# Performance work log

Measured on AMD Instinct MI355X. Metric: run time of the kernel, lower is better.

## Reference

```python
import jax, jax.numpy as jnp
import numpy as np

D_MODEL = 1024
N_HEADS = 16
D_K = D_MODEL // N_HEADS
MAX_REL = 128
SCALE = 1.0 / np.sqrt(D_K)
TEMP = 1.0


def setup_inputs() -> dict:
    key = jax.random.key(0)
    ks = jax.random.split(key, 12)
    B, S = 4, 1024
    inp = {
        "query": jax.random.normal(ks[0], (B, S, D_MODEL), jnp.float32),
        "key": jax.random.normal(ks[1], (B, S, D_MODEL), jnp.float32),
        "value": jax.random.normal(ks[2], (B, S, D_MODEL), jnp.float32),
        "mask": jnp.ones((B, S), jnp.int32),
        "w_q": jax.random.normal(ks[3], (D_MODEL, D_MODEL), jnp.float32) * 0.03,
        "b_q": jnp.zeros((D_MODEL,), jnp.float32),
        "w_k": jax.random.normal(ks[4], (D_MODEL, D_MODEL), jnp.float32) * 0.03,
        "b_k": jnp.zeros((D_MODEL,), jnp.float32),
        "w_v": jax.random.normal(ks[5], (D_MODEL, D_MODEL), jnp.float32) * 0.03,
        "b_v": jnp.zeros((D_MODEL,), jnp.float32),
        "w_o": jax.random.normal(ks[6], (D_MODEL, D_MODEL), jnp.float32) * 0.03,
        "b_o": jnp.zeros((D_MODEL,), jnp.float32),
        "rel_k": jax.random.normal(ks[7], (2 * MAX_REL + 1, D_K), jnp.float32),
        "rel_v": jax.random.normal(ks[8], (2 * MAX_REL + 1, D_K), jnp.float32),
    }
    return inp


def _relative_positions(seq_len):
    pos = jnp.arange(seq_len)
    rel = pos[None, :] - pos[:, None]  # [S, S]
    return jnp.clip(rel, -MAX_REL, MAX_REL) + MAX_REL


def reference(query, key, value, mask, w_q, b_q, w_k, b_k, w_v, b_v, w_o, b_o, rel_k, rel_v):
    B, S, _ = query.shape
    # projections (torch Linear: x @ W.T + b)
    Q = (query @ w_q.T + b_q).reshape(B, S, N_HEADS, D_K).transpose(0, 2, 1, 3)  # [B,H,S,d]
    K = (key @ w_k.T + b_k).reshape(B, S, N_HEADS, D_K).transpose(0, 2, 1, 3)
    V = (value @ w_v.T + b_v).reshape(B, S, N_HEADS, D_K).transpose(0, 2, 1, 3)

    scores = jnp.einsum("bhld,bhrd->bhlr", Q, K) * SCALE  # [B,H,S,S]

    rel_idx = _relative_positions(S)                      # [S,S] int
    rpk = rel_k[rel_idx]                                  # [S,S,d]
    scores = scores + jnp.einsum("bhld,lrd->bhlr", Q, rpk)

    scores = scores / TEMP
    m = mask[:, None, None, :]                            # [B,1,1,S]
    scores = jnp.where(m == 0, -1e9, scores)

    attn = jax.nn.softmax(scores, axis=-1)                # [B,H,S,S]
    context = jnp.einsum("bhlr,bhrd->bhld", attn, V)
    rpv = rel_v[rel_idx]                                  # [S,S,d]
    context = context + jnp.einsum("bhlr,lrd->bhld", attn, rpv)

    context = context.transpose(0, 2, 1, 3).reshape(B, S, D_MODEL)
    out = context @ w_o.T + b_o
    return out
```

## Files before the change

kernel.cpp:

```cpp
#include <hip/hip_runtime.h>
#include <hip/hip_bf16.h>

#define S_LEN  1024
#define DMODEL 1024
#define NHEADS 16
#define DK     64
#define SCALE  0.125f

typedef __bf16 bf16x8_t __attribute__((ext_vector_type(8)));
typedef __bf16 bf16x4_t __attribute__((ext_vector_type(4)));
typedef float  f32x4_t  __attribute__((ext_vector_type(4)));

#define MFMA16(A, B, C) __builtin_amdgcn_mfma_f32_16x16x32_bf16((A), (B), (C), 0, 0, 0)

__device__ __forceinline__ void async16(const void* g, void* l) {
    __builtin_amdgcn_global_load_lds(
        (const __attribute__((address_space(1))) unsigned int*)g,
        (__attribute__((address_space(3))) unsigned int*)l, 16, 0, 0);
}

__global__ __launch_bounds__(256) void cast_all_kernel(
    const float* __restrict__ q, const float* __restrict__ k, const float* __restrict__ v,
    const float* __restrict__ wq, const float* __restrict__ wk,
    const float* __restrict__ wv, const float* __restrict__ wo,
    const float* __restrict__ relk, const float* __restrict__ relv,
    __bf16* __restrict__ Xbf, __bf16* __restrict__ Wall,
    __bf16* __restrict__ relkp, __bf16* __restrict__ rvT,
    __bf16* __restrict__ Wqlo)
{
    const long i = (long)blockIdx.x * 256 + threadIdx.x;
    if (i < 3145728) {
        const int z   = (int)(i >> 20);
        const long rem = i & 1048575;
        const float4 s = ((const float4*)(z == 0 ? q : (z == 1 ? k : v)))[rem];
        bf16x4_t h;
        h[0] = (__bf16)s.x; h[1] = (__bf16)s.y; h[2] = (__bf16)s.z; h[3] = (__bf16)s.w;
        *(bf16x4_t*)(Xbf + ((size_t)z << 22) + rem * 4) = h;
    } else if (i < 3145728 + 1048576) {
        const long wi = i - 3145728;
        const int z   = (int)(wi >> 18);
        const long rem = wi & 262143;
        const float* src = (z == 0) ? wq : (z == 1) ? wk : (z == 2) ? wv : wo;
        const float4 s = ((const float4*)src)[rem];
        const float xs[4] = {s.x, s.y, s.z, s.w};
        bf16x4_t h;
        #pragma unroll
        for (int t = 0; t < 4; ++t) h[t] = (__bf16)xs[t];
        *(bf16x4_t*)(Wall + ((size_t)z << 20) + rem * 4) = h;
        if (z == 0) {
            bf16x4_t l;
            #pragma unroll
            for (int t = 0; t < 4; ++t) l[t] = (__bf16)(xs[t] - (float)h[t]);
            *(bf16x4_t*)(Wqlo + rem * 4) = l;
        }
    } else if (i < 3145728 + 1048576 + 4352) {
        const long ri = i - (3145728 + 1048576);
        const int j  = (int)(ri >> 4);
        const int d4 = (int)(ri & 15) * 4;
        bf16x4_t h, l;
        if (j < 257) {
            const float4 s = *(const float4*)(relk + j * 64 + d4);
            const float xs[4] = {s.x, s.y, s.z, s.w};
            #pragma unroll
            for (int t = 0; t < 4; ++t) {
                h[t] = (__bf16)xs[t];
                l[t] = (__bf16)(xs[t] - (float)h[t]);
            }
        } else {
            #pragma unroll
            for (int t = 0; t < 4; ++t) { h[t] = (__bf16)0.f; l[t] = (__bf16)0.f; }
        }
        *(bf16x4_t*)(relkp + j * 64 + d4) = h;
        *(bf16x4_t*)(relkp + 17408 + j * 64 + d4) = l;
    } else if (i < 3145728 + 1048576 + 4352 + 4608) {
        const long ri = i - (3145728 + 1048576 + 4352);
        const int d  = (int)(ri / 72);
        const int j4 = (int)(ri % 72) * 4;
        bf16x4_t o;
        #pragma unroll
        for (int t = 0; t < 4; ++t) {
            const int j = j4 + t;
            o[t] = (j < 257) ? (__bf16)relv[j * 64 + d] : (__bf16)0.f;
        }
        *(bf16x4_t*)(rvT + d * 288 + j4) = o;
    }
}

__device__ __forceinline__ void gemm128_core(
    const __bf16* __restrict__ A, const __bf16* __restrict__ W,
    __bf16* As, __bf16* Ws, f32x4_t acc[4][4])
{
    const int tid  = threadIdx.x;
    const int lane = tid & 63;
    const int quad = lane >> 4;
    const int l15  = lane & 15;
    const int wid  = tid >> 6;
    const int wm = wid >> 1, wn = wid & 1;

    for (int kt = 0; kt < 32; ++kt) {
        #pragma unroll
        for (int r = 0; r < 2; ++r) {
            const int c = r * 256 + tid;
            const int row = c >> 2, kb = c & 3;
            async16(A + row * 1024 + kt * 32 + kb * 8, As + c * 8);
            async16(W + row * 1024 + kt * 32 + kb * 8, Ws + c * 8);
        }
        __syncthreads();
        bf16x8_t af[4], wf[4];
        #pragma unroll
        for (int i = 0; i < 4; ++i) {
            af[i] = *(const bf16x8_t*)(As + (wm * 64 + i * 16 + l15) * 32 + quad * 8);
            wf[i] = *(const bf16x8_t*)(Ws + (wn * 64 + i * 16 + l15) * 32 + quad * 8);
        }
        #pragma unroll
        for (int i = 0; i < 4; ++i)
            #pragma unroll
            for (int j = 0; j < 4; ++j)
                acc[i][j] = MFMA16(af[i], wf[j], acc[i][j]);
        __syncthreads();
    }
}

__global__ __launch_bounds__(256) void gemm_qkv_kernel(
    const __bf16* __restrict__ Xbf, const __bf16* __restrict__ Wall,
    const __bf16* __restrict__ Wqlo,
    const float* __restrict__ bq, const float* __restrict__ bk, const float* __restrict__ bv,
    __bf16* __restrict__ QKVh)
{
    __shared__ __bf16 As[4096], Ws[4096];
    const int z = blockIdx.z;
    const __bf16* A = Xbf + (size_t)z * 4194304 + (size_t)blockIdx.y * 131072;
    const __bf16* W = Wall + (size_t)z * 1048576 + (size_t)blockIdx.x * 131072;
    f32x4_t acc[4][4];
    #pragma unroll
    for (int i = 0; i < 4; ++i)
        #pragma unroll
        for (int j = 0; j < 4; ++j)
            acc[i][j] = (f32x4_t){0.f, 0.f, 0.f, 0.f};

    gemm128_core(A, W, As, Ws, acc);
    if (z == 0)
        gemm128_core(A, Wqlo + (size_t)blockIdx.x * 131072, As, Ws, acc);

    const int tid = threadIdx.x, lane = tid & 63, quad = lane >> 4, l15 = lane & 15;
    const int wid = tid >> 6, wm = wid >> 1, wn = wid & 1;
    const int m0 = blockIdx.y * 128 + wm * 64;
    const int n0 = blockIdx.x * 128 + wn * 64;
    const float* bias = (z == 0) ? bq : ((z == 1) ? bk : bv);
    __bf16* dst = QKVh + (size_t)z * 4194304;

    if (z < 2) {
        #pragma unroll
        for (int j = 0; j < 4; ++j) {
            const int n = n0 + j * 16 + l15;
            const float bn = bias[n];
            #pragma unroll
            for (int i = 0; i < 4; ++i) {
                #pragma unroll
                for (int v = 0; v < 4; ++v) {
                    const int m = m0 + i * 16 + quad * 4 + v;
                    dst[((((m >> 10) * 16 + (n >> 6)) << 16)) + ((m & 1023) << 6) + (n & 63)]
                        = (__bf16)(acc[i][j][v] + bn);
                }
            }
        }
    } else {
        #pragma unroll
        for (int j = 0; j < 4; ++j) {
            const int n = n0 + j * 16 + l15;
            const float bn = bias[n];
            #pragma unroll
            for (int i = 0; i < 4; ++i) {
                const int m = m0 + i * 16 + quad * 4;
                bf16x4_t pk;
                #pragma unroll
                for (int v = 0; v < 4; ++v) pk[v] = (__bf16)(acc[i][j][v] + bn);
                const int s = m & 1023, d = n & 63;
                const size_t idx = (((size_t)((m >> 10) * 16 + (n >> 6))) << 16)
                                 + (size_t)(s >> 5) * 2048 + d * 32 + (s & 31);
                *(bf16x4_t*)(dst + idx) = pk;
            }
        }
    }
}

__global__ __launch_bounds__(256) void gemm_out_kernel(
    const __bf16* __restrict__ ctx, const __bf16* __restrict__ Wo,
    const float* __restrict__ bo, float* __restrict__ out)
{
    __shared__ __bf16 As[4096], Ws[4096];
    const __bf16* A = ctx + (size_t)blockIdx.y * 131072;
    const __bf16* W = Wo + (size_t)blockIdx.x * 131072;
    f32x4_t acc[4][4];
    #pragma unroll
    for (int i = 0; i < 4; ++i)
        #pragma unroll
        for (int j = 0; j < 4; ++j)
            acc[i][j] = (f32x4_t){0.f, 0.f, 0.f, 0.f};
    gemm128_core(A, W, As, Ws, acc);

    const int tid = threadIdx.x, lane = tid & 63, quad = lane >> 4, l15 = lane & 15;
    const int wid = tid >> 6, wm = wid >> 1, wn = wid & 1;
    const int m0 = blockIdx.y * 128 + wm * 64;
    const int n0 = blockIdx.x * 128 + wn * 64;
    #pragma unroll
    for (int j = 0; j < 4; ++j) {
        const int n = n0 + j * 16 + l15;
        const float bn = bo[n];
        #pragma unroll
        for (int i = 0; i < 4; ++i)
            #pragma unroll
            for (int v = 0; v < 4; ++v) {
                const int m = m0 + i * 16 + quad * 4 + v;
                out[(size_t)m * 1024 + n] = acc[i][j][v] + bn;
            }
    }
}

__global__ __launch_bounds__(256) void qrel_kernel(
    const __bf16* __restrict__ Qh, const __bf16* __restrict__ relkp,
    _Float16* __restrict__ qrelG)
{
    const int tid = threadIdx.x, lane = tid & 63, wid = tid >> 6;
    const int quad = lane >> 4, l15 = lane & 15;
    const int bh = blockIdx.y;
    const int l0 = blockIdx.x * 64 + wid * 16;
    const __bf16* Qbase = Qh + (size_t)bh * 65536;
    const __bf16* relk_hi = relkp;
    const __bf16* relk_lo = relkp + 17408;
    const bf16x8_t aq0 = *(const bf16x8_t*)(Qbase + (l0 + l15) * 64 + quad * 8);
    const bf16x8_t aq1 = *(const bf16x8_t*)(Qbase + (l0 + l15) * 64 + 32 + quad * 8);
    _Float16* out = qrelG + ((size_t)bh * 1024 + l0) * 272;
    for (int nt = 0; nt < 17; ++nt) {
        const int j = nt * 16 + l15;
        const bf16x8_t h0  = *(const bf16x8_t*)(relk_hi + j * 64 + quad * 8);
        const bf16x8_t h1  = *(const bf16x8_t*)(relk_hi + j * 64 + 32 + quad * 8);
        const bf16x8_t lo0 = *(const bf16x8_t*)(relk_lo + j * 64 + quad * 8);
        const bf16x8_t lo1 = *(const bf16x8_t*)(relk_lo + j * 64 + 32 + quad * 8);
        f32x4_t c = (f32x4_t){0.f, 0.f, 0.f, 0.f};
        c = MFMA16(aq0, lo0, c);
        c = MFMA16(aq1, lo1, c);
        c = MFMA16(aq0, h0, c);
        c = MFMA16(aq1, h1, c);
        #pragma unroll
        for (int v = 0; v < 4; ++v)
            out[(quad * 4 + v) * 272 + j] = (_Float16)c[v];
    }
}

__global__ __launch_bounds__(256, 4) void attn_far_kernel(
    const __bf16* __restrict__ Qh, const __bf16* __restrict__ Kh,
    const __bf16* __restrict__ Vt, const _Float16* __restrict__ qrelG,
    const int* __restrict__ mask, const float* __restrict__ relv,
    float* __restrict__ OfarG, float* __restrict__ rsG)
{
    __shared__ __align__(16) __bf16 Ks[2048];
    __shared__ __align__(16) __bf16 Vs[2048];
    __shared__ __align__(16) __bf16 p_s[4][16][40];

    const int tid = threadIdx.x, lane = tid & 63, wid = tid >> 6;
    const int quad = lane >> 4, l15 = lane & 15;
    const int lin = blockIdx.x;
    const int slot = lin >> 3;
    const int bh = (lin & 7) + 8 * (slot >> 4);
    const int chunk = slot & 15;
    const int b = bh >> 4;
    const int t0w = chunk * 4 + wid;
    const int l0 = t0w * 16;

    const __bf16* Qbase = Qh + (size_t)bh * 65536;
    const __bf16* Kbase = Kh + (size_t)bh * 65536;
    const __bf16* Vbase = Vt + (size_t)bh * 65536;
    const _Float16* qr  = qrelG + ((size_t)bh * 1024 + l0) * 272;
    const int* maskb = mask + b * 1024;

    const bf16x8_t aq0 = *(const bf16x8_t*)(Qbase + (l0 + l15) * 64 + quad * 8);
    const bf16x8_t aq1 = *(const bf16x8_t*)(Qbase + (l0 + l15) * 64 + 32 + quad * 8);

    float c0[4], c1[4];
    #pragma unroll
    for (int v = 0; v < 4; ++v) {
        c0[v] = (float)qr[(quad * 4 + v) * 272 + 0];
        c1[v] = (float)qr[(quad * 4 + v) * 272 + 256];
    }

    int gK[2], lK[2], gV[2], lV[2];
    #pragma unroll
    for (int ii = 0; ii < 2; ++ii) {
        const int ch = (wid & 1) * 128 + ii * 64 + lane;
        {
            const int r = ch >> 3, p = ch & 7, g = p ^ (r & 7);
            gK[ii] = r * 64 + g * 8;
            lK[ii] = ch * 8;
        }
        {
            const int d = ch >> 2, p = ch & 3, g = p ^ ((d >> 1) & 3);
            gV[ii] = d * 32 + g * 8;
            lV[ii] = ch * 8;
        }
    }

    f32x4_t o[4];
    #pragma unroll
    for (int dt = 0; dt < 4; ++dt) o[dt] = (f32x4_t){0.f, 0.f, 0.f, 0.f};
    float e0[4] = {0.f, 0.f, 0.f, 0.f};
    float e1[4] = {0.f, 0.f, 0.f, 0.f};

    for (int pc = 0; pc < 32; ++pc) {
        const int rb0 = pc * 32;
        if (wid < 2) {
            #pragma unroll
            for (int ii = 0; ii < 2; ++ii)
                async16(Kbase + rb0 * 64 + gK[ii], Ks + lK[ii]);
        } else {
            #pragma unroll
            for (int ii = 0; ii < 2; ++ii)
                async16(Vbase + pc * 2048 + gV[ii], Vs + lV[ii]);
        }
        __syncthreads();

        const int tI0 = pc * 2;
        const bool far0 = (tI0 <= t0w - 9) || (tI0 >= t0w + 9);
        const bool far1 = (tI0 + 1 <= t0w - 9) || (tI0 + 1 >= t0w + 9);
        if (far0 || far1) {
            #pragma unroll
            for (int sl = 0; sl < 2; ++sl) {
                const bool isFar = sl ? far1 : far0;
                if (isFar) {
                    const int R = sl * 16 + l15;
                    const bf16x8_t kb0 =
                        *(const bf16x8_t*)(Ks + R * 64 + (quad ^ (R & 7)) * 8);
                    const bf16x8_t kb1 =
                        *(const bf16x8_t*)(Ks + R * 64 + (((quad + 4) ^ (R & 7))) * 8);
                    f32x4_t s = (f32x4_t){0.f, 0.f, 0.f, 0.f};
                    s = MFMA16(aq0, kb0, s);
                    s = MFMA16(aq1, kb1, s);
                    const float madd = (maskb[rb0 + R] == 0) ? -1.0e9f : 0.f;
                    const bool isLo = (tI0 + sl < t0w);
                    #pragma unroll
                    for (int v = 0; v < 4; ++v) {
                        const float cc = isLo ? c0[v] : c1[v];
                        const float p = __expf(fmaf(s[v], SCALE, cc) + madd);
                        const __bf16 pb = (__bf16)p;
                        const float pf = (float)pb;
                        if (isLo) e0[v] += pf; else e1[v] += pf;
                        p_s[wid][quad * 4 + v][sl * 16 + l15] = pb;
                    }
                } else {
                    #pragma unroll
                    for (int v = 0; v < 4; ++v)
                        p_s[wid][quad * 4 + v][sl * 16 + l15] = (__bf16)0.f;
                }
            }
            const bf16x8_t pa = *(const bf16x8_t*)(&p_s[wid][l15][quad * 8]);
            #pragma unroll
            for (int dt = 0; dt < 4; ++dt) {
                const int D = dt * 16 + l15;
                const bf16x8_t vb =
                    *(const bf16x8_t*)(Vs + D * 32 + ((quad ^ ((D >> 1) & 3))) * 8);
                o[dt] = MFMA16(pa, vb, o[dt]);
            }
        }
        __syncthreads();
    }

    #pragma unroll
    for (int v = 0; v < 4; ++v)
        #pragma unroll
        for (int mm = 1; mm < 16; mm <<= 1) {
            e0[v] += __shfl_xor(e0[v], mm, 64);
            e1[v] += __shfl_xor(e1[v], mm, 64);
        }

    float* Od = OfarG + ((size_t)bh * 1024 + l0) * 64;
    #pragma unroll
    for (int dt = 0; dt < 4; ++dt) {
        const int d = dt * 16 + l15;
        const float rv0   = relv[d];
        const float rv256 = relv[256 * 64 + d];
        #pragma unroll
        for (int v = 0; v < 4; ++v)
            Od[(quad * 4 + v) * 64 + d] = o[dt][v] + e0[v] * rv0 + e1[v] * rv256;
    }
    if (l15 == 0) {
        #pragma unroll
        for (int v = 0; v < 4; ++v)
            rsG[bh * 1024 + l0 + quad * 4 + v] = e0[v] + e1[v];
    }
}

__global__ __launch_bounds__(64, 4) void attn_band_kernel(
    const __bf16* __restrict__ Qh, const __bf16* __restrict__ Kh,
    const __bf16* __restrict__ Vt, const _Float16* __restrict__ qrelG,
    const __bf16* __restrict__ rvT, const int* __restrict__ mask,
    const float* __restrict__ OfarG, const float* __restrict__ rsG,
    __bf16* __restrict__ ctx)
{
    __shared__ __align__(16) __bf16 w_s[16][288];
    __shared__ __align__(16) __bf16 p_s[16][40];

    const int lane = threadIdx.x & 63;
    const int quad = lane >> 4, l15 = lane & 15;
    const int lin = blockIdx.x;
    const int slot = lin >> 3;
    const int bh = (lin & 7) + 8 * (slot >> 6);
    const int t0 = slot & 63, l0 = t0 * 16;
    const int b = bh >> 4;

    const __bf16* Qbase = Qh + (size_t)bh * 65536;
    const __bf16* Kbase = Kh + (size_t)bh * 65536;
    const __bf16* Vbase = Vt + (size_t)bh * 65536;
    const _Float16* qr  = qrelG + ((size_t)bh * 1024 + l0) * 272;

    {
        uint4* wz = (uint4*)&w_s[0][0];
        for (int t = lane; t < 576; t += 64) wz[t] = (uint4){0u, 0u, 0u, 0u};
    }

    const bf16x8_t aq0 = *(const bf16x8_t*)(Qbase + (l0 + l15) * 64 + quad * 8);
    const bf16x8_t aq1 = *(const bf16x8_t*)(Qbase + (l0 + l15) * 64 + 32 + quad * 8);

    const int tstart = t0 > 8 ? t0 - 8 : 0;
    const int tend   = t0 < 55 ? t0 + 8 : 63;
    const int nb = tend - tstart + 1;

    f32x4_t o[4];
    #pragma unroll
    for (int dt = 0; dt < 4; ++dt) o[dt] = (f32x4_t){0.f, 0.f, 0.f, 0.f};
    float rowsum[4] = {0.f, 0.f, 0.f, 0.f};
    float e0[4] = {0.f, 0.f, 0.f, 0.f};
    float e1[4] = {0.f, 0.f, 0.f, 0.f};

    for (int m = 0; m < nb; m += 2) {
        const int rbA = (tstart + m) * 16;
        const bool hasB = (m + 1 < nb);
        const int rbB = hasB ? rbA + 16 : rbA;
        #pragma unroll
        for (int slotn = 0; slotn < 2; ++slotn) {
            if (slotn == 1 && !hasB) {
                #pragma unroll
                for (int v = 0; v < 4; ++v)
                    p_s[quad * 4 + v][16 + l15] = (__bf16)0.f;
                break;
            }
            const int rb = slotn ? rbB : rbA;
            const int r = rb + l15;
            const bf16x8_t kb0 = *(const bf16x8_t*)(Kbase + r * 64 + quad * 8);
            const bf16x8_t kb1 = *(const bf16x8_t*)(Kbase + r * 64 + 32 + quad * 8);
            f32x4_t s = (f32x4_t){0.f, 0.f, 0.f, 0.f};
            s = MFMA16(aq0, kb0, s);
            s = MFMA16(aq1, kb1, s);
            const float madd = (mask[b * 1024 + r] == 0) ? -1.0e9f : 0.f;
            #pragma unroll
            for (int v = 0; v < 4; ++v) {
                const int lrow = quad * 4 + v;
                const int dd = r - (l0 + lrow);
                int j = dd + 128; j = j < 0 ? 0 : (j > 256 ? 256 : j);
                const float bias = (float)qr[lrow * 272 + j];
                const float p = __expf(fmaf(s[v], SCALE, bias) + madd);
                const __bf16 pb = (__bf16)p;
                const float pf = (float)pb;
                rowsum[v] += pf;
                p_s[lrow][slotn * 16 + l15] = pb;
                if (j == 0)        e0[v] += pf;
                else if (j == 256) e1[v] += pf;
                else               w_s[lrow][j] = pb;
            }
        }
        const bf16x8_t pa = *(const bf16x8_t*)(&p_s[l15][quad * 8]);
        const int rr = (quad < 2) ? (rbA + quad * 8) : (rbB + (quad - 2) * 8);
        #pragma unroll
        for (int dt = 0; dt < 4; ++dt) {
            const bf16x8_t vb = *(const bf16x8_t*)(
                Vbase + (rr >> 5) * 2048 + (dt * 16 + l15) * 32 + (rr & 31));
            o[dt] = MFMA16(pa, vb, o[dt]);
        }
    }

    #pragma unroll
    for (int v = 0; v < 4; ++v) {
        #pragma unroll
        for (int mm = 1; mm < 16; mm <<= 1) {
            rowsum[v] += __shfl_xor(rowsum[v], mm, 64);
            e0[v]     += __shfl_xor(e0[v], mm, 64);
            e1[v]     += __shfl_xor(e1[v], mm, 64);
        }
    }
    if (l15 == 0) {
        #pragma unroll
        for (int v = 0; v < 4; ++v) {
            w_s[quad * 4 + v][0]   = (__bf16)e0[v];
            w_s[quad * 4 + v][256] = (__bf16)e1[v];
        }
    }

    for (int kc = 0; kc < 9; ++kc) {
        const bf16x8_t wa = *(const bf16x8_t*)(&w_s[l15][kc * 32 + quad * 8]);
        #pragma unroll
        for (int dt = 0; dt < 4; ++dt) {
            const bf16x8_t rb =
                *(const bf16x8_t*)(rvT + (dt * 16 + l15) * 288 + kc * 32 + quad * 8);
            o[dt] = MFMA16(wa, rb, o[dt]);
        }
    }

    float rinv[4];
    #pragma unroll
    for (int v = 0; v < 4; ++v)
        rinv[v] = 1.f / (rowsum[v] + rsG[bh * 1024 + l0 + quad * 4 + v]);
    const float* Od = OfarG + ((size_t)bh * 1024 + l0) * 64;
    const int h = bh & 15;
    #pragma unroll
    for (int dt = 0; dt < 4; ++dt)
        #pragma unroll
        for (int v = 0; v < 4; ++v) {
            const int lrow = quad * 4 + v;
            const float val = (o[dt][v] + Od[lrow * 64 + dt * 16 + l15]) * rinv[v];
            ctx[((size_t)b * 1024 + l0 + lrow) * 1024 + h * 64 + dt * 16 + l15]
                = (__bf16)val;
        }
}

extern "C" void kernel_launch(void* const* d_in, const int* in_sizes, int n_in,
                              void* d_out, int out_size, void* d_ws, size_t ws_size,
                              hipStream_t stream)
{
    const float* q    = (const float*)d_in[0];
    const float* k    = (const float*)d_in[1];
    const float* v    = (const float*)d_in[2];
    const int*   mask = (const int*)  d_in[3];
    const float* wq   = (const float*)d_in[4];
    const float* bq   = (const float*)d_in[5];
    const float* wk   = (const float*)d_in[6];
    const float* bk   = (const float*)d_in[7];
    const float* wv   = (const float*)d_in[8];
    const float* bv   = (const float*)d_in[9];
    const float* wo   = (const float*)d_in[10];
    const float* bo   = (const float*)d_in[11];
    const float* relk = (const float*)d_in[12];
    const float* relv = (const float*)d_in[13];

    __bf16* Xbf   = (__bf16*)d_ws;
    __bf16* Xgap  = Xbf   + 12582912;
    __bf16* Wqlo  = Xgap  + 4194304;
    __bf16* Wall  = Wqlo  + 1048576;
    __bf16* QKVh  = Wall  + 4194304;
    __bf16* ctx   = QKVh  + 12582912;
    __bf16* relkp = ctx   + 4194304;
    __bf16* rvT   = relkp + 34816;
    float*  OfarG = (float*)(rvT + 18432);
    float*  rsG   = OfarG + 4194304;
    _Float16* qrelG = (_Float16*)d_ws;

    cast_all_kernel<<<16419, 256, 0, stream>>>(q, k, v, wq, wk, wv, wo, relk, relv,
                                               Xbf, Wall, relkp, rvT, Wqlo);
    gemm_qkv_kernel<<<dim3(8, 32, 3), 256, 0, stream>>>(Xbf, Wall, Wqlo,
                                                        bq, bk, bv, QKVh);
    qrel_kernel<<<dim3(16, 64), 256, 0, stream>>>(QKVh, relkp, qrelG);
    attn_far_kernel<<<1024, 256, 0, stream>>>(QKVh, QKVh + 4194304,
                                              QKVh + 2 * 4194304, qrelG, mask,
                                              relv, OfarG, rsG);
    attn_band_kernel<<<4096, 64, 0, stream>>>(QKVh, QKVh + 4194304,
                                              QKVh + 2 * 4194304, qrelG,
                                              rvT, mask, OfarG, rsG, ctx);
    gemm_out_kernel<<<dim3(8, 32, 1), 256, 0, stream>>>(ctx, Wall + 3 * 1048576,
                                                        bo, (float*)d_out);
}
```

Before: 350.2 us.

## Fuse Q·relK bias computation into attention kernels and prefetch band K/V

Removes the separate qrel kernel and its global fp16 buffer. attn_far now computes only the two edge bias columns with a few MFMAs, and attn_band computes the full 272-column bias table into shared memory. The band loop also software-prefetches the next K/V/mask tiles into registers. Edge-weight contributions are applied directly with relv instead of through the w_s MFMA. The fused version repeats the bias GEMM per band block and adds LDS and registers, so the launch bound is relaxed to 2.

```diff
diff --git a/kernel.cpp b/kernel.cpp
--- a/kernel.cpp
+++ b/kernel.cpp
@@ -217,40 +217,9 @@
     }
 }
 
-__global__ __launch_bounds__(256) void qrel_kernel(
-    const __bf16* __restrict__ Qh, const __bf16* __restrict__ relkp,
-    _Float16* __restrict__ qrelG)
-{
-    const int tid = threadIdx.x, lane = tid & 63, wid = tid >> 6;
-    const int quad = lane >> 4, l15 = lane & 15;
-    const int bh = blockIdx.y;
-    const int l0 = blockIdx.x * 64 + wid * 16;
-    const __bf16* Qbase = Qh + (size_t)bh * 65536;
-    const __bf16* relk_hi = relkp;
-    const __bf16* relk_lo = relkp + 17408;
-    const bf16x8_t aq0 = *(const bf16x8_t*)(Qbase + (l0 + l15) * 64 + quad * 8);
-    const bf16x8_t aq1 = *(const bf16x8_t*)(Qbase + (l0 + l15) * 64 + 32 + quad * 8);
-    _Float16* out = qrelG + ((size_t)bh * 1024 + l0) * 272;
-    for (int nt = 0; nt < 17; ++nt) {
-        const int j = nt * 16 + l15;
-        const bf16x8_t h0  = *(const bf16x8_t*)(relk_hi + j * 64 + quad * 8);
-        const bf16x8_t h1  = *(const bf16x8_t*)(relk_hi + j * 64 + 32 + quad * 8);
-        const bf16x8_t lo0 = *(const bf16x8_t*)(relk_lo + j * 64 + quad * 8);
-        const bf16x8_t lo1 = *(const bf16x8_t*)(relk_lo + j * 64 + 32 + quad * 8);
-        f32x4_t c = (f32x4_t){0.f, 0.f, 0.f, 0.f};
-        c = MFMA16(aq0, lo0, c);
-        c = MFMA16(aq1, lo1, c);
-        c = MFMA16(aq0, h0, c);
-        c = MFMA16(aq1, h1, c);
-        #pragma unroll
-        for (int v = 0; v < 4; ++v)
-            out[(quad * 4 + v) * 272 + j] = (_Float16)c[v];
-    }
-}
-
 __global__ __launch_bounds__(256, 4) void attn_far_kernel(
     const __bf16* __restrict__ Qh, const __bf16* __restrict__ Kh,
-    const __bf16* __restrict__ Vt, const _Float16* __restrict__ qrelG,
+    const __bf16* __restrict__ Vt, const __bf16* __restrict__ relkp,
     const int* __restrict__ mask, const float* __restrict__ relv,
     float* __restrict__ OfarG, float* __restrict__ rsG)
 {
@@ -271,17 +240,28 @@
     const __bf16* Qbase = Qh + (size_t)bh * 65536;
     const __bf16* Kbase = Kh + (size_t)bh * 65536;
     const __bf16* Vbase = Vt + (size_t)bh * 65536;
-    const _Float16* qr  = qrelG + ((size_t)bh * 1024 + l0) * 272;
     const int* maskb = mask + b * 1024;
 
     const bf16x8_t aq0 = *(const bf16x8_t*)(Qbase + (l0 + l15) * 64 + quad * 8);
     const bf16x8_t aq1 = *(const bf16x8_t*)(Qbase + (l0 + l15) * 64 + 32 + quad * 8);
 
     float c0[4], c1[4];
-    #pragma unroll
-    for (int v = 0; v < 4; ++v) {
-        c0[v] = (float)qr[(quad * 4 + v) * 272 + 0];
-        c1[v] = (float)qr[(quad * 4 + v) * 272 + 256];
+    {
+        const int jr = (l15 == 1) ? 256 : 0;
+        const bf16x8_t bh0 = *(const bf16x8_t*)(relkp + jr * 64 + quad * 8);
+        const bf16x8_t bh1 = *(const bf16x8_t*)(relkp + jr * 64 + 32 + quad * 8);
+        const bf16x8_t bl0 = *(const bf16x8_t*)(relkp + 17408 + jr * 64 + quad * 8);
+        const bf16x8_t bl1 = *(const bf16x8_t*)(relkp + 17408 + jr * 64 + 32 + quad * 8);
+        f32x4_t cr = (f32x4_t){0.f, 0.f, 0.f, 0.f};
+        cr = MFMA16(aq0, bl0, cr);
+        cr = MFMA16(aq1, bl1, cr);
+        cr = MFMA16(aq0, bh0, cr);
+        cr = MFMA16(aq1, bh1, cr);
+        #pragma unroll
+        for (int v = 0; v < 4; ++v) {
+            c0[v] = __shfl(cr[v], (lane & 48), 64);
+            c1[v] = __shfl(cr[v], (lane & 48) | 1, 64);
+        }
     }
 
     int gK[2], lK[2], gV[2], lV[2];
@@ -389,15 +369,17 @@
     }
 }
 
-__global__ __launch_bounds__(64, 4) void attn_band_kernel(
+__global__ __launch_bounds__(64, 2) void attn_band_kernel(
     const __bf16* __restrict__ Qh, const __bf16* __restrict__ Kh,
-    const __bf16* __restrict__ Vt, const _Float16* __restrict__ qrelG,
+    const __bf16* __restrict__ Vt, const __bf16* __restrict__ relkp,
     const __bf16* __restrict__ rvT, const int* __restrict__ mask,
+    const float* __restrict__ relv,
     const float* __restrict__ OfarG, const float* __restrict__ rsG,
     __bf16* __restrict__ ctx)
 {
-    __shared__ __align__(16) __bf16 w_s[16][288];
+    __shared__ __align__(16) __bf16 w_s[16][272];
     __shared__ __align__(16) __bf16 p_s[16][40];
+    __shared__ __align__(16) _Float16 qr_s[16][276];
 
     const int lane = threadIdx.x & 63;
     const int quad = lane >> 4, l15 = lane & 15;
@@ -410,15 +392,36 @@
     const __bf16* Qbase = Qh + (size_t)bh * 65536;
     const __bf16* Kbase = Kh + (size_t)bh * 65536;
     const __bf16* Vbase = Vt + (size_t)bh * 65536;
-    const _Float16* qr  = qrelG + ((size_t)bh * 1024 + l0) * 272;
+    const int* maskb = mask + b * 1024;
 
     {
         uint4* wz = (uint4*)&w_s[0][0];
-        for (int t = lane; t < 576; t += 64) wz[t] = (uint4){0u, 0u, 0u, 0u};
+        for (int t = lane; t < 544; t += 64) wz[t] = (uint4){0u, 0u, 0u, 0u};
     }
 
     const bf16x8_t aq0 = *(const bf16x8_t*)(Qbase + (l0 + l15) * 64 + quad * 8);
     const bf16x8_t aq1 = *(const bf16x8_t*)(Qbase + (l0 + l15) * 64 + 32 + quad * 8);
+
+    {
+        const __bf16* rhi = relkp;
+        const __bf16* rlo = relkp + 17408;
+        #pragma unroll 4
+        for (int nt = 0; nt < 17; ++nt) {
+            const int j = nt * 16 + l15;
+            const bf16x8_t h0 = *(const bf16x8_t*)(rhi + j * 64 + quad * 8);
+            const bf16x8_t h1 = *(const bf16x8_t*)(rhi + j * 64 + 32 + quad * 8);
+            const bf16x8_t g0 = *(const bf16x8_t*)(rlo + j * 64 + quad * 8);
+            const bf16x8_t g1 = *(const bf16x8_t*)(rlo + j * 64 + 32 + quad * 8);
+            f32x4_t c = (f32x4_t){0.f, 0.f, 0.f, 0.f};
+            c = MFMA16(aq0, g0, c);
+            c = MFMA16(aq1, g1, c);
+            c = MFMA16(aq0, h0, c);
+            c = MFMA16(aq1, h1, c);
+            #pragma unroll
+            for (int v = 0; v < 4; ++v)
+                qr_s[quad * 4 + v][j] = (_Float16)c[v];
+        }
+    }
 
     const int tstart = t0 > 8 ? t0 - 8 : 0;
     const int tend   = t0 < 55 ? t0 + 8 : 63;
@@ -431,49 +434,92 @@
     float e0[4] = {0.f, 0.f, 0.f, 0.f};
     float e1[4] = {0.f, 0.f, 0.f, 0.f};
 
+    bf16x8_t kb[2][2], vb[4];
+    int rbA = tstart * 16;
+    int rbB = rbA + 16;
+    int mA, mB;
+    {
+        #pragma unroll
+        for (int sl = 0; sl < 2; ++sl) {
+            const int r = (sl ? rbB : rbA) + l15;
+            kb[sl][0] = *(const bf16x8_t*)(Kbase + r * 64 + quad * 8);
+            kb[sl][1] = *(const bf16x8_t*)(Kbase + r * 64 + 32 + quad * 8);
+        }
+        const int rr = (quad < 2) ? (rbA + quad * 8) : (rbB + (quad - 2) * 8);
+        #pragma unroll
+        for (int dt = 0; dt < 4; ++dt)
+            vb[dt] = *(const bf16x8_t*)(Vbase + (rr >> 5) * 2048
+                                        + (dt * 16 + l15) * 32 + (rr & 31));
+        mA = maskb[rbA + l15];
+        mB = maskb[rbB + l15];
+    }
+
     for (int m = 0; m < nb; m += 2) {
-        const int rbA = (tstart + m) * 16;
         const bool hasB = (m + 1 < nb);
-        const int rbB = hasB ? rbA + 16 : rbA;
+        const bool hasN = (m + 2 < nb);
+        bf16x8_t kbn[2][2], vbn[4];
+        int mAn = 0, mBn = 0, rbAn = 0, rbBn = 0;
+        if (hasN) {
+            rbAn = (tstart + m + 2) * 16;
+            rbBn = (m + 3 < nb) ? rbAn + 16 : rbAn;
+            #pragma unroll
+            for (int sl = 0; sl < 2; ++sl) {
+                const int r = (sl ? rbBn : rbAn) + l15;
+                kbn[sl][0] = *(const bf16x8_t*)(Kbase + r * 64 + quad * 8);
+                kbn[sl][1] = *(const bf16x8_t*)(Kbase + r * 64 + 32 + quad * 8);
+            }
+            const int rr = (quad < 2) ? (rbAn + quad * 8) : (rbBn + (quad - 2) * 8);
+            #pragma unroll
+            for (int dt = 0; dt < 4; ++dt)
+                vbn[dt] = *(const bf16x8_t*)(Vbase + (rr >> 5) * 2048
+                                             + (dt * 16 + l15) * 32 + (rr & 31));
+            mAn = maskb[rbAn + l15];
+            mBn = maskb[rbBn + l15];
+        }
+
         #pragma unroll
         for (int slotn = 0; slotn < 2; ++slotn) {
             if (slotn == 1 && !hasB) {
                 #pragma unroll
                 for (int v = 0; v < 4; ++v)
                     p_s[quad * 4 + v][16 + l15] = (__bf16)0.f;
-                break;
-            }
-            const int rb = slotn ? rbB : rbA;
-            const int r = rb + l15;
-            const bf16x8_t kb0 = *(const bf16x8_t*)(Kbase + r * 64 + quad * 8);
-            const bf16x8_t kb1 = *(const bf16x8_t*)(Kbase + r * 64 + 32 + quad * 8);
-            f32x4_t s = (f32x4_t){0.f, 0.f, 0.f, 0.f};
-            s = MFMA16(aq0, kb0, s);
-            s = MFMA16(aq1, kb1, s);
-            const float madd = (mask[b * 1024 + r] == 0) ? -1.0e9f : 0.f;
-            #pragma unroll
-            for (int v = 0; v < 4; ++v) {
-                const int lrow = quad * 4 + v;
-                const int dd = r - (l0 + lrow);
-                int j = dd + 128; j = j < 0 ? 0 : (j > 256 ? 256 : j);
-                const float bias = (float)qr[lrow * 272 + j];
-                const float p = __expf(fmaf(s[v], SCALE, bias) + madd);
-                const __bf16 pb = (__bf16)p;
-                const float pf = (float)pb;
-                rowsum[v] += pf;
-                p_s[lrow][slotn * 16 + l15] = pb;
-                if (j == 0)        e0[v] += pf;
-                else if (j == 256) e1[v] += pf;
-                else               w_s[lrow][j] = pb;
+            } else {
+                const int rb = slotn ? rbB : rbA;
+                const int r = rb + l15;
+                f32x4_t s = (f32x4_t){0.f, 0.f, 0.f, 0.f};
+                s = MFMA16(aq0, kb[slotn][0], s);
+                s = MFMA16(aq1, kb[slotn][1], s);
+                const float madd = ((slotn ? mB : mA) == 0) ? -1.0e9f : 0.f;
+                #pragma unroll
+                for (int v = 0; v < 4; ++v) {
+                    const int lrow = quad * 4 + v;
+                    const int dd = r - (l0 + lrow);
+                    int j = dd + 128; j = j < 0 ? 0 : (j > 256 ? 256 : j);
+                    const float bias = (float)qr_s[lrow][j];
+                    const float p = __expf(fmaf(s[v], SCALE, bias) + madd);
+                    const __bf16 pb = (__bf16)p;
+                    const float pf = (float)pb;
+                    rowsum[v] += pf;
+                    p_s[lrow][slotn * 16 + l15] = pb;
+                    if (j == 0)        e0[v] += pf;
+                    else if (j == 256) e1[v] += pf;
+                    else               w_s[lrow][j] = pb;
+                }
             }
         }
         const bf16x8_t pa = *(const bf16x8_t*)(&p_s[l15][quad * 8]);
-        const int rr = (quad < 2) ? (rbA + quad * 8) : (rbB + (quad - 2) * 8);
-        #pragma unroll
-        for (int dt = 0; dt < 4; ++dt) {
-            const bf16x8_t vb = *(const bf16x8_t*)(
-                Vbase + (rr >> 5) * 2048 + (dt * 16 + l15) * 32 + (rr & 31));
-            o[dt] = MFMA16(pa, vb, o[dt]);
+        #pragma unroll
+        for (int dt = 0; dt < 4; ++dt)
+            o[dt] = MFMA16(pa, vb[dt], o[dt]);
+        if (hasN) {
+            #pragma unroll
+            for (int sl = 0; sl < 2; ++sl) {
+                kb[sl][0] = kbn[sl][0];
+                kb[sl][1] = kbn[sl][1];
+            }
+            #pragma unroll
+            for (int dt = 0; dt < 4; ++dt) vb[dt] = vbn[dt];
+            mA = mAn; mB = mBn; rbA = rbAn; rbB = rbBn;
         }
     }
 
@@ -486,15 +532,8 @@
             e1[v]     += __shfl_xor(e1[v], mm, 64);
         }
     }
-    if (l15 == 0) {
-        #pragma unroll
-        for (int v = 0; v < 4; ++v) {
-            w_s[quad * 4 + v][0]   = (__bf16)e0[v];
-            w_s[quad * 4 + v][256] = (__bf16)e1[v];
-        }
-    }
-
-    for (int kc = 0; kc < 9; ++kc) {
+
+    for (int kc = 0; kc < 8; ++kc) {
         const bf16x8_t wa = *(const bf16x8_t*)(&w_s[l15][kc * 32 + quad * 8]);
         #pragma unroll
         for (int dt = 0; dt < 4; ++dt) {
@@ -511,14 +550,18 @@
     const float* Od = OfarG + ((size_t)bh * 1024 + l0) * 64;
     const int h = bh & 15;
     #pragma unroll
-    for (int dt = 0; dt < 4; ++dt)
+    for (int dt = 0; dt < 4; ++dt) {
+        const int d = dt * 16 + l15;
+        const float rv0   = relv[d];
+        const float rv256 = relv[256 * 64 + d];
         #pragma unroll
         for (int v = 0; v < 4; ++v) {
             const int lrow = quad * 4 + v;
-            const float val = (o[dt][v] + Od[lrow * 64 + dt * 16 + l15]) * rinv[v];
-            ctx[((size_t)b * 1024 + l0 + lrow) * 1024 + h * 64 + dt * 16 + l15]
-                = (__bf16)val;
-        }
+            const float val = (o[dt][v] + e0[v] * rv0 + e1[v] * rv256
+                               + Od[lrow * 64 + d]) * rinv[v];
+            ctx[((size_t)b * 1024 + l0 + lrow) * 1024 + h * 64 + d] = (__bf16)val;
+        }
+    }
 }
 
 extern "C" void kernel_launch(void* const* d_in, const int* in_sizes, int n_in,
@@ -550,19 +593,17 @@
     __bf16* rvT   = relkp + 34816;
     float*  OfarG = (float*)(rvT + 18432);
     float*  rsG   = OfarG + 4194304;
-    _Float16* qrelG = (_Float16*)d_ws;
 
     cast_all_kernel<<<16419, 256, 0, stream>>>(q, k, v, wq, wk, wv, wo, relk, relv,
                                                Xbf, Wall, relkp, rvT, Wqlo);
     gemm_qkv_kernel<<<dim3(8, 32, 3), 256, 0, stream>>>(Xbf, Wall, Wqlo,
                                                         bq, bk, bv, QKVh);
-    qrel_kernel<<<dim3(16, 64), 256, 0, stream>>>(QKVh, relkp, qrelG);
     attn_far_kernel<<<1024, 256, 0, stream>>>(QKVh, QKVh + 4194304,
-                                              QKVh + 2 * 4194304, qrelG, mask,
+                                              QKVh + 2 * 4194304, relkp, mask,
                                               relv, OfarG, rsG);
     attn_band_kernel<<<4096, 64, 0, stream>>>(QKVh, QKVh + 4194304,
-                                              QKVh + 2 * 4194304, qrelG,
-                                              rvT, mask, OfarG, rsG, ctx);
+                                              QKVh + 2 * 4194304, relkp,
+                                              rvT, mask, relv, OfarG, rsG, ctx);
     gemm_out_kernel<<<dim3(8, 32, 1), 256, 0, stream>>>(ctx, Wall + 3 * 1048576,
                                                         bo, (float*)d_out);
 }
```

Measured after the change: 319.1 us. 1.1x faster.

## Fuse qrel, far and band attention kernels into one double-buffered kernel

Applied to the files above, without the earlier changes.

Replaces the separate qrel precompute, far-field attention and band attention kernels with a single kernel that computes relative-key biases on the fly with MFMA for near tiles and handles the band's rel_v contribution in the same pass. This removes the qrelG, OfarG and rsG global round trips and two kernel launches. K/V tiles are now double-buffered with async loads, and blocks shrink to 128 threads (two waves). The cost is extra MFMA work per band tile for bias recomputation, more LDS per block, and heavier per-wave work.

```diff
diff --git a/kernel.cpp b/kernel.cpp
--- a/kernel.cpp
+++ b/kernel.cpp
@@ -217,77 +217,37 @@
     }
 }
 
-__global__ __launch_bounds__(256) void qrel_kernel(
-    const __bf16* __restrict__ Qh, const __bf16* __restrict__ relkp,
-    _Float16* __restrict__ qrelG)
-{
-    const int tid = threadIdx.x, lane = tid & 63, wid = tid >> 6;
-    const int quad = lane >> 4, l15 = lane & 15;
-    const int bh = blockIdx.y;
-    const int l0 = blockIdx.x * 64 + wid * 16;
-    const __bf16* Qbase = Qh + (size_t)bh * 65536;
-    const __bf16* relk_hi = relkp;
-    const __bf16* relk_lo = relkp + 17408;
-    const bf16x8_t aq0 = *(const bf16x8_t*)(Qbase + (l0 + l15) * 64 + quad * 8);
-    const bf16x8_t aq1 = *(const bf16x8_t*)(Qbase + (l0 + l15) * 64 + 32 + quad * 8);
-    _Float16* out = qrelG + ((size_t)bh * 1024 + l0) * 272;
-    for (int nt = 0; nt < 17; ++nt) {
-        const int j = nt * 16 + l15;
-        const bf16x8_t h0  = *(const bf16x8_t*)(relk_hi + j * 64 + quad * 8);
-        const bf16x8_t h1  = *(const bf16x8_t*)(relk_hi + j * 64 + 32 + quad * 8);
-        const bf16x8_t lo0 = *(const bf16x8_t*)(relk_lo + j * 64 + quad * 8);
-        const bf16x8_t lo1 = *(const bf16x8_t*)(relk_lo + j * 64 + 32 + quad * 8);
-        f32x4_t c = (f32x4_t){0.f, 0.f, 0.f, 0.f};
-        c = MFMA16(aq0, lo0, c);
-        c = MFMA16(aq1, lo1, c);
-        c = MFMA16(aq0, h0, c);
-        c = MFMA16(aq1, h1, c);
-        #pragma unroll
-        for (int v = 0; v < 4; ++v)
-            out[(quad * 4 + v) * 272 + j] = (_Float16)c[v];
-    }
-}
-
-__global__ __launch_bounds__(256, 4) void attn_far_kernel(
+__global__ __launch_bounds__(128, 2) void attn_fused_kernel(
     const __bf16* __restrict__ Qh, const __bf16* __restrict__ Kh,
-    const __bf16* __restrict__ Vt, const _Float16* __restrict__ qrelG,
-    const int* __restrict__ mask, const float* __restrict__ relv,
-    float* __restrict__ OfarG, float* __restrict__ rsG)
-{
-    __shared__ __align__(16) __bf16 Ks[2048];
-    __shared__ __align__(16) __bf16 Vs[2048];
-    __shared__ __align__(16) __bf16 p_s[4][16][40];
+    const __bf16* __restrict__ Vt, const __bf16* __restrict__ relkp,
+    const __bf16* __restrict__ rvT, const int* __restrict__ mask,
+    const float* __restrict__ relv, __bf16* __restrict__ ctx)
+{
+    __shared__ __align__(16) __bf16 Ks[2][2048];
+    __shared__ __align__(16) __bf16 Vs[2][2048];
+    __shared__ __align__(16) __bf16 p_s[2][16][40];
+    __shared__ __align__(16) __bf16 w_s[2][16][272];
 
     const int tid = threadIdx.x, lane = tid & 63, wid = tid >> 6;
     const int quad = lane >> 4, l15 = lane & 15;
     const int lin = blockIdx.x;
     const int slot = lin >> 3;
-    const int bh = (lin & 7) + 8 * (slot >> 4);
-    const int chunk = slot & 15;
+    const int bh = (lin & 7) + 8 * (slot >> 5);
+    const int chunk = slot & 31;
     const int b = bh >> 4;
-    const int t0w = chunk * 4 + wid;
+    const int t0w = chunk * 2 + wid;
     const int l0 = t0w * 16;
 
     const __bf16* Qbase = Qh + (size_t)bh * 65536;
     const __bf16* Kbase = Kh + (size_t)bh * 65536;
     const __bf16* Vbase = Vt + (size_t)bh * 65536;
-    const _Float16* qr  = qrelG + ((size_t)bh * 1024 + l0) * 272;
     const int* maskb = mask + b * 1024;
-
-    const bf16x8_t aq0 = *(const bf16x8_t*)(Qbase + (l0 + l15) * 64 + quad * 8);
-    const bf16x8_t aq1 = *(const bf16x8_t*)(Qbase + (l0 + l15) * 64 + 32 + quad * 8);
-
-    float c0[4], c1[4];
-    #pragma unroll
-    for (int v = 0; v < 4; ++v) {
-        c0[v] = (float)qr[(quad * 4 + v) * 272 + 0];
-        c1[v] = (float)qr[(quad * 4 + v) * 272 + 256];
-    }
-
-    int gK[2], lK[2], gV[2], lV[2];
-    #pragma unroll
-    for (int ii = 0; ii < 2; ++ii) {
-        const int ch = (wid & 1) * 128 + ii * 64 + lane;
+    const __bf16* rlo = relkp + 17408;
+
+    int gK[4], lK[4], gV[4], lV[4];
+    #pragma unroll
+    for (int ii = 0; ii < 4; ++ii) {
+        const int ch = ii * 64 + lane;
         {
             const int r = ch >> 3, p = ch & 7, g = p ^ (r & 7);
             gK[ii] = r * 64 + g * 8;
@@ -300,225 +260,187 @@
         }
     }
 
+    if (wid == 0) {
+        #pragma unroll
+        for (int ii = 0; ii < 4; ++ii)
+            async16(Kbase + gK[ii], &Ks[0][0] + lK[ii]);
+    } else {
+        #pragma unroll
+        for (int ii = 0; ii < 4; ++ii)
+            async16(Vbase + gV[ii], &Vs[0][0] + lV[ii]);
+    }
+
+    const bf16x8_t aq0 = *(const bf16x8_t*)(Qbase + (l0 + l15) * 64 + quad * 8);
+    const bf16x8_t aq1 = *(const bf16x8_t*)(Qbase + (l0 + l15) * 64 + 32 + quad * 8);
+
+    float c0[4], c1[4];
+    {
+        const int jr = (l15 == 1) ? 256 : 0;
+        const bf16x8_t bh0 = *(const bf16x8_t*)(relkp + jr * 64 + quad * 8);
+        const bf16x8_t bh1 = *(const bf16x8_t*)(relkp + jr * 64 + 32 + quad * 8);
+        const bf16x8_t bl0 = *(const bf16x8_t*)(rlo + jr * 64 + quad * 8);
+        const bf16x8_t bl1 = *(const bf16x8_t*)(rlo + jr * 64 + 32 + quad * 8);
+        f32x4_t cr = (f32x4_t){0.f, 0.f, 0.f, 0.f};
+        cr = MFMA16(aq0, bl0, cr);
+        cr = MFMA16(aq1, bl1, cr);
+        cr = MFMA16(aq0, bh0, cr);
+        cr = MFMA16(aq1, bh1, cr);
+        #pragma unroll
+        for (int v = 0; v < 4; ++v) {
+            c0[v] = __shfl(cr[v], (lane & 48), 64);
+            c1[v] = __shfl(cr[v], (lane & 48) | 1, 64);
+        }
+    }
+
+    {
+        uint4* wz = (uint4*)&w_s[wid][0][0];
+        for (int t = lane; t < 544; t += 64) wz[t] = (uint4){0u, 0u, 0u, 0u};
+    }
+
     f32x4_t o[4];
     #pragma unroll
     for (int dt = 0; dt < 4; ++dt) o[dt] = (f32x4_t){0.f, 0.f, 0.f, 0.f};
+    float rowsum[4] = {0.f, 0.f, 0.f, 0.f};
     float e0[4] = {0.f, 0.f, 0.f, 0.f};
     float e1[4] = {0.f, 0.f, 0.f, 0.f};
 
+    __syncthreads();
+
     for (int pc = 0; pc < 32; ++pc) {
+        const int cur = pc & 1;
+        if (pc + 1 < 32) {
+            if (wid == 0) {
+                #pragma unroll
+                for (int ii = 0; ii < 4; ++ii)
+                    async16(Kbase + (pc + 1) * 2048 + gK[ii], &Ks[cur ^ 1][0] + lK[ii]);
+            } else {
+                #pragma unroll
+                for (int ii = 0; ii < 4; ++ii)
+                    async16(Vbase + (pc + 1) * 2048 + gV[ii], &Vs[cur ^ 1][0] + lV[ii]);
+            }
+        }
+
         const int rb0 = pc * 32;
-        if (wid < 2) {
-            #pragma unroll
-            for (int ii = 0; ii < 2; ++ii)
-                async16(Kbase + rb0 * 64 + gK[ii], Ks + lK[ii]);
-        } else {
-            #pragma unroll
-            for (int ii = 0; ii < 2; ++ii)
-                async16(Vbase + pc * 2048 + gV[ii], Vs + lV[ii]);
+        const int tI0 = pc * 2;
+        #pragma unroll
+        for (int sl = 0; sl < 2; ++sl) {
+            const int tI = tI0 + sl;
+            const int dist = tI - t0w;
+            const int R = sl * 16 + l15;
+            const bf16x8_t kb0 =
+                *(const bf16x8_t*)(&Ks[cur][0] + R * 64 + (quad ^ (R & 7)) * 8);
+            const bf16x8_t kb1 =
+                *(const bf16x8_t*)(&Ks[cur][0] + R * 64 + (((quad + 4) ^ (R & 7))) * 8);
+            f32x4_t s = (f32x4_t){0.f, 0.f, 0.f, 0.f};
+            s = MFMA16(aq0, kb0, s);
+            s = MFMA16(aq1, kb1, s);
+            const float madd = (maskb[rb0 + R] == 0) ? -1.0e9f : 0.f;
+
+            if (dist <= -9 || dist >= 9) {
+                const bool isLo = dist < 0;
+                #pragma unroll
+                for (int v = 0; v < 4; ++v) {
+                    const float cc = isLo ? c0[v] : c1[v];
+                    const float p = __expf(fmaf(s[v], SCALE, cc) + madd);
+                    const __bf16 pb = (__bf16)p;
+                    const float pf = (float)pb;
+                    rowsum[v] += pf;
+                    if (isLo) e0[v] += pf; else e1[v] += pf;
+                    p_s[wid][quad * 4 + v][sl * 16 + l15] = pb;
+                }
+            } else {
+                const int base = dist * 16 + 128;
+                int ra = base - 15 + l15;
+                ra = ra < 0 ? 0 : (ra > 256 ? 256 : ra);
+                int rb2 = base + 1 + l15;
+                rb2 = rb2 > 256 ? 256 : rb2;
+                const bf16x8_t hA0 = *(const bf16x8_t*)(relkp + ra * 64 + quad * 8);
+                const bf16x8_t hA1 = *(const bf16x8_t*)(relkp + ra * 64 + 32 + quad * 8);
+                const bf16x8_t lA0 = *(const bf16x8_t*)(rlo + ra * 64 + quad * 8);
+                const bf16x8_t lA1 = *(const bf16x8_t*)(rlo + ra * 64 + 32 + quad * 8);
+                const bf16x8_t hB0 = *(const bf16x8_t*)(relkp + rb2 * 64 + quad * 8);
+                const bf16x8_t hB1 = *(const bf16x8_t*)(relkp + rb2 * 64 + 32 + quad * 8);
+                const bf16x8_t lB0 = *(const bf16x8_t*)(rlo + rb2 * 64 + quad * 8);
+                const bf16x8_t lB1 = *(const bf16x8_t*)(rlo + rb2 * 64 + 32 + quad * 8);
+                f32x4_t qbA = (f32x4_t){0.f, 0.f, 0.f, 0.f};
+                f32x4_t qbB = (f32x4_t){0.f, 0.f, 0.f, 0.f};
+                qbA = MFMA16(aq0, lA0, qbA);
+                qbA = MFMA16(aq1, lA1, qbA);
+                qbA = MFMA16(aq0, hA0, qbA);
+                qbA = MFMA16(aq1, hA1, qbA);
+                qbB = MFMA16(aq0, lB0, qbB);
+                qbB = MFMA16(aq1, lB1, qbB);
+                qbB = MFMA16(aq0, hB0, qbB);
+                qbB = MFMA16(aq1, hB1, qbB);
+                #pragma unroll
+                for (int v = 0; v < 4; ++v) {
+                    const int lrow = quad * 4 + v;
+                    const int c = l15 + 15 - lrow;
+                    const int src = (lane & 48) | (c & 15);
+                    const float bA = __shfl(qbA[v], src, 64);
+                    const float bB = __shfl(qbB[v], src, 64);
+                    const float qbv = (c & 16) ? bB : bA;
+                    const int j = base + l15 - lrow;
+                    const float bias = (j < 0) ? c0[v] : ((j > 256) ? c1[v] : qbv);
+                    const float p = __expf(fmaf(s[v], SCALE, bias) + madd);
+                    const __bf16 pb = (__bf16)p;
+                    const float pf = (float)pb;
+                    rowsum[v] += pf;
+                    p_s[wid][lrow][sl * 16 + l15] = pb;
+                    if (j <= 0)        e0[v] += pf;
+                    else if (j >= 256) e1[v] += pf;
+                    else               w_s[wid][lrow][j] = pb;
+                }
+            }
+        }
+        const bf16x8_t pa = *(const bf16x8_t*)(&p_s[wid][l15][quad * 8]);
+        #pragma unroll
+        for (int dt = 0; dt < 4; ++dt) {
+            const int D = dt * 16 + l15;
+            const bf16x8_t vb =
+                *(const bf16x8_t*)(&Vs[cur][0] + D * 32 + ((quad ^ ((D >> 1) & 3))) * 8);
+            o[dt] = MFMA16(pa, vb, o[dt]);
         }
         __syncthreads();
-
-        const int tI0 = pc * 2;
-        const bool far0 = (tI0 <= t0w - 9) || (tI0 >= t0w + 9);
-        const bool far1 = (tI0 + 1 <= t0w - 9) || (tI0 + 1 >= t0w + 9);
-        if (far0 || far1) {
-            #pragma unroll
-            for (int sl = 0; sl < 2; ++sl) {
-                const bool isFar = sl ? far1 : far0;
-                if (isFar) {
-                    const int R = sl * 16 + l15;
-                    const bf16x8_t kb0 =
-                        *(const bf16x8_t*)(Ks + R * 64 + (quad ^ (R & 7)) * 8);
-                    const bf16x8_t kb1 =
-                        *(const bf16x8_t*)(Ks + R * 64 + (((quad + 4) ^ (R & 7))) * 8);
-                    f32x4_t s = (f32x4_t){0.f, 0.f, 0.f, 0.f};
-                    s = MFMA16(aq0, kb0, s);
-                    s = MFMA16(aq1, kb1, s);
-                    const float madd = (maskb[rb0 + R] == 0) ? -1.0e9f : 0.f;
-                    const bool isLo = (tI0 + sl < t0w);
-                    #pragma unroll
-                    for (int v = 0; v < 4; ++v) {
-                        const float cc = isLo ? c0[v] : c1[v];
-                        const float p = __expf(fmaf(s[v], SCALE, cc) + madd);
-                        const __bf16 pb = (__bf16)p;
-                        const float pf = (float)pb;
-                        if (isLo) e0[v] += pf; else e1[v] += pf;
-                        p_s[wid][quad * 4 + v][sl * 16 + l15] = pb;
-                    }
-                } else {
-                    #pragma unroll
-                    for (int v = 0; v < 4; ++v)
-                        p_s[wid][quad * 4 + v][sl * 16 + l15] = (__bf16)0.f;
-                }
-            }
-            const bf16x8_t pa = *(const bf16x8_t*)(&p_s[wid][l15][quad * 8]);
-            #pragma unroll
-            for (int dt = 0; dt < 4; ++dt) {
-                const int D = dt * 16 + l15;
-                const bf16x8_t vb =
-                    *(const bf16x8_t*)(Vs + D * 32 + ((quad ^ ((D >> 1) & 3))) * 8);
-                o[dt] = MFMA16(pa, vb, o[dt]);
-            }
-        }
-        __syncthreads();
-    }
-
+    }
+
+    for (int kc = 0; kc < 8; ++kc) {
+        const bf16x8_t wa = *(const bf16x8_t*)(&w_s[wid][l15][kc * 32 + quad * 8]);
+        #pragma unroll
+        for (int dt = 0; dt < 4; ++dt) {
+            const bf16x8_t rb =
+                *(const bf16x8_t*)(rvT + (dt * 16 + l15) * 288 + kc * 32 + quad * 8);
+            o[dt] = MFMA16(wa, rb, o[dt]);
+        }
+    }
+
+    #pragma unroll
+    for (int v = 0; v < 4; ++v) {
+        #pragma unroll
+        for (int mm = 1; mm < 16; mm <<= 1) {
+            rowsum[v] += __shfl_xor(rowsum[v], mm, 64);
+            e0[v]     += __shfl_xor(e0[v], mm, 64);
+            e1[v]     += __shfl_xor(e1[v], mm, 64);
+        }
+    }
+
+    float rinv[4];
     #pragma unroll
     for (int v = 0; v < 4; ++v)
-        #pragma unroll
-        for (int mm = 1; mm < 16; mm <<= 1) {
-            e0[v] += __shfl_xor(e0[v], mm, 64);
-            e1[v] += __shfl_xor(e1[v], mm, 64);
-        }
-
-    float* Od = OfarG + ((size_t)bh * 1024 + l0) * 64;
+        rinv[v] = 1.f / rowsum[v];
+    const int h = bh & 15;
     #pragma unroll
     for (int dt = 0; dt < 4; ++dt) {
         const int d = dt * 16 + l15;
         const float rv0   = relv[d];
         const float rv256 = relv[256 * 64 + d];
         #pragma unroll
-        for (int v = 0; v < 4; ++v)
-            Od[(quad * 4 + v) * 64 + d] = o[dt][v] + e0[v] * rv0 + e1[v] * rv256;
-    }
-    if (l15 == 0) {
-        #pragma unroll
-        for (int v = 0; v < 4; ++v)
-            rsG[bh * 1024 + l0 + quad * 4 + v] = e0[v] + e1[v];
-    }
-}
-
-__global__ __launch_bounds__(64, 4) void attn_band_kernel(
-    const __bf16* __restrict__ Qh, const __bf16* __restrict__ Kh,
-    const __bf16* __restrict__ Vt, const _Float16* __restrict__ qrelG,
-    const __bf16* __restrict__ rvT, const int* __restrict__ mask,
-    const float* __restrict__ OfarG, const float* __restrict__ rsG,
-    __bf16* __restrict__ ctx)
-{
-    __shared__ __align__(16) __bf16 w_s[16][288];
-    __shared__ __align__(16) __bf16 p_s[16][40];
-
-    const int lane = threadIdx.x & 63;
-    const int quad = lane >> 4, l15 = lane & 15;
-    const int lin = blockIdx.x;
-    const int slot = lin >> 3;
-    const int bh = (lin & 7) + 8 * (slot >> 6);
-    const int t0 = slot & 63, l0 = t0 * 16;
-    const int b = bh >> 4;
-
-    const __bf16* Qbase = Qh + (size_t)bh * 65536;
-    const __bf16* Kbase = Kh + (size_t)bh * 65536;
-    const __bf16* Vbase = Vt + (size_t)bh * 65536;
-    const _Float16* qr  = qrelG + ((size_t)bh * 1024 + l0) * 272;
-
-    {
-        uint4* wz = (uint4*)&w_s[0][0];
-        for (int t = lane; t < 576; t += 64) wz[t] = (uint4){0u, 0u, 0u, 0u};
-    }
-
-    const bf16x8_t aq0 = *(const bf16x8_t*)(Qbase + (l0 + l15) * 64 + quad * 8);
-    const bf16x8_t aq1 = *(const bf16x8_t*)(Qbase + (l0 + l15) * 64 + 32 + quad * 8);
-
-    const int tstart = t0 > 8 ? t0 - 8 : 0;
-    const int tend   = t0 < 55 ? t0 + 8 : 63;
-    const int nb = tend - tstart + 1;
-
-    f32x4_t o[4];
-    #pragma unroll
-    for (int dt = 0; dt < 4; ++dt) o[dt] = (f32x4_t){0.f, 0.f, 0.f, 0.f};
-    float rowsum[4] = {0.f, 0.f, 0.f, 0.f};
-    float e0[4] = {0.f, 0.f, 0.f, 0.f};
-    float e1[4] = {0.f, 0.f, 0.f, 0.f};
-
-    for (int m = 0; m < nb; m += 2) {
-        const int rbA = (tstart + m) * 16;
-        const bool hasB = (m + 1 < nb);
-        const int rbB = hasB ? rbA + 16 : rbA;
-        #pragma unroll
-        for (int slotn = 0; slotn < 2; ++slotn) {
-            if (slotn == 1 && !hasB) {
-                #pragma unroll
-                for (int v = 0; v < 4; ++v)
-                    p_s[quad * 4 + v][16 + l15] = (__bf16)0.f;
-                break;
-            }
-            const int rb = slotn ? rbB : rbA;
-            const int r = rb + l15;
-            const bf16x8_t kb0 = *(const bf16x8_t*)(Kbase + r * 64 + quad * 8);
-            const bf16x8_t kb1 = *(const bf16x8_t*)(Kbase + r * 64 + 32 + quad * 8);
-            f32x4_t s = (f32x4_t){0.f, 0.f, 0.f, 0.f};
-            s = MFMA16(aq0, kb0, s);
-            s = MFMA16(aq1, kb1, s);
-            const float madd = (mask[b * 1024 + r] == 0) ? -1.0e9f : 0.f;
-            #pragma unroll
-            for (int v = 0; v < 4; ++v) {
-                const int lrow = quad * 4 + v;
-                const int dd = r - (l0 + lrow);
-                int j = dd + 128; j = j < 0 ? 0 : (j > 256 ? 256 : j);
-                const float bias = (float)qr[lrow * 272 + j];
-                const float p = __expf(fmaf(s[v], SCALE, bias) + madd);
-                const __bf16 pb = (__bf16)p;
-                const float pf = (float)pb;
-                rowsum[v] += pf;
-                p_s[lrow][slotn * 16 + l15] = pb;
-                if (j == 0)        e0[v] += pf;
-                else if (j == 256) e1[v] += pf;
-                else               w_s[lrow][j] = pb;
-            }
-        }
-        const bf16x8_t pa = *(const bf16x8_t*)(&p_s[l15][quad * 8]);
-        const int rr = (quad < 2) ? (rbA + quad * 8) : (rbB + (quad - 2) * 8);
-        #pragma unroll
-        for (int dt = 0; dt < 4; ++dt) {
-            const bf16x8_t vb = *(const bf16x8_t*)(
-                Vbase + (rr >> 5) * 2048 + (dt * 16 + l15) * 32 + (rr & 31));
-            o[dt] = MFMA16(pa, vb, o[dt]);
-        }
-    }
-
-    #pragma unroll
-    for (int v = 0; v < 4; ++v) {
-        #pragma unroll
-        for (int mm = 1; mm < 16; mm <<= 1) {
-            rowsum[v] += __shfl_xor(rowsum[v], mm, 64);
-            e0[v]     += __shfl_xor(e0[v], mm, 64);
-            e1[v]     += __shfl_xor(e1[v], mm, 64);
-        }
-    }
-    if (l15 == 0) {
-        #pragma unroll
-        for (int v = 0; v < 4; ++v) {
-            w_s[quad * 4 + v][0]   = (__bf16)e0[v];
-            w_s[quad * 4 + v][256] = (__bf16)e1[v];
-        }
-    }
-
-    for (int kc = 0; kc < 9; ++kc) {
-        const bf16x8_t wa = *(const bf16x8_t*)(&w_s[l15][kc * 32 + quad * 8]);
-        #pragma unroll
-        for (int dt = 0; dt < 4; ++dt) {
-            const bf16x8_t rb =
-                *(const bf16x8_t*)(rvT + (dt * 16 + l15) * 288 + kc * 32 + quad * 8);
-            o[dt] = MFMA16(wa, rb, o[dt]);
-        }
-    }
-
-    float rinv[4];
-    #pragma unroll
-    for (int v = 0; v < 4; ++v)
-        rinv[v] = 1.f / (rowsum[v] + rsG[bh * 1024 + l0 + quad * 4 + v]);
-    const float* Od = OfarG + ((size_t)bh * 1024 + l0) * 64;
-    const int h = bh & 15;
-    #pragma unroll
-    for (int dt = 0; dt < 4; ++dt)
-        #pragma unroll
         for (int v = 0; v < 4; ++v) {
             const int lrow = quad * 4 + v;
-            const float val = (o[dt][v] + Od[lrow * 64 + dt * 16 + l15]) * rinv[v];
-            ctx[((size_t)b * 1024 + l0 + lrow) * 1024 + h * 64 + dt * 16 + l15]
-                = (__bf16)val;
-        }
+            const float val = (o[dt][v] + e0[v] * rv0 + e1[v] * rv256) * rinv[v];
+            ctx[((size_t)b * 1024 + l0 + lrow) * 1024 + h * 64 + d] = (__bf16)val;
+        }
+    }
 }
 
 extern "C" void kernel_launch(void* const* d_in, const int* in_sizes, int n_in,
@@ -548,21 +470,14 @@
     __bf16* ctx   = QKVh  + 12582912;
     __bf16* relkp = ctx   + 4194304;
     __bf16* rvT   = relkp + 34816;
-    float*  OfarG = (float*)(rvT + 18432);
-    float*  rsG   = OfarG + 4194304;
-    _Float16* qrelG = (_Float16*)d_ws;
 
     cast_all_kernel<<<16419, 256, 0, stream>>>(q, k, v, wq, wk, wv, wo, relk, relv,
                                                Xbf, Wall, relkp, rvT, Wqlo);
     gemm_qkv_kernel<<<dim3(8, 32, 3), 256, 0, stream>>>(Xbf, Wall, Wqlo,
                                                         bq, bk, bv, QKVh);
-    qrel_kernel<<<dim3(16, 64), 256, 0, stream>>>(QKVh, relkp, qrelG);
-    attn_far_kernel<<<1024, 256, 0, stream>>>(QKVh, QKVh + 4194304,
-                                              QKVh + 2 * 4194304, qrelG, mask,
-                                              relv, OfarG, rsG);
-    attn_band_kernel<<<4096, 64, 0, stream>>>(QKVh, QKVh + 4194304,
-                                              QKVh + 2 * 4194304, qrelG,
-                                              rvT, mask, OfarG, rsG, ctx);
+    attn_fused_kernel<<<2048, 128, 0, stream>>>(QKVh, QKVh + 4194304,
+                                                QKVh + 2 * 4194304, relkp,
+                                                rvT, mask, relv, ctx);
     gemm_out_kernel<<<dim3(8, 32, 1), 256, 0, stream>>>(ctx, Wall + 3 * 1048576,
                                                         bo, (float*)d_out);
 }
```

Result: faster. 340.8 us (-2.7%).
